# Kernel optimization log

Measured on AMD Instinct MI355X. Metric: run time of the kernel, lower is better.

Reference implementation:

```python
import jax, jax.numpy as jnp
import numpy as np
from jax import lax

IN_CH, OUT_CH, K, STYLE_DIM = 512, 512, 3, 512
B, H, W = 16, 64, 64
SCALE = 1.0 / np.sqrt(IN_CH * K * K).astype(np.float32)
EPS = 1e-8


def setup_inputs() -> dict:
    key = jax.random.key(0)
    k1, k2, k3, k4 = jax.random.split(key, 4)
    return {
        "x": jax.random.normal(k1, (B, IN_CH, H, W), dtype=jnp.float32),
        "style": jax.random.normal(k2, (B, STYLE_DIM), dtype=jnp.float32),
        "weight": jax.random.normal(k3, (1, OUT_CH, IN_CH, K, K), dtype=jnp.float32),
        "mod_w": jax.random.normal(k4, (IN_CH, STYLE_DIM), dtype=jnp.float32) / np.sqrt(STYLE_DIM),
        "mod_b": jnp.ones((IN_CH,), dtype=jnp.float32),
    }


def reference(x, style, weight, mod_w, mod_b):
    b, cin, h, w = x.shape
    out_ch = weight.shape[1]
    k = weight.shape[-1]
    pad = k // 2
    # style projection: (B, in_channel)
    s = style @ mod_w.T + mod_b
    # modulated weight: (B, out, in, k, k)
    wmod = SCALE * weight * s[:, None, :, None, None]
    # demodulation: rsqrt of sum of squares over (in, kh, kw)
    demod = lax.rsqrt(jnp.sum(wmod * wmod, axis=(2, 3, 4)) + EPS)
    wmod = wmod * demod[:, :, None, None, None]
    # grouped conv with groups = batch
    wflat = wmod.reshape(b * out_ch, cin, k, k)
    xin = x.reshape(1, b * cin, h, w)
    out = lax.conv_general_dilated(
        xin, wflat,
        window_strides=(1, 1),
        padding=[(pad, pad), (pad, pad)],
        dimension_numbers=("NCHW", "OIHW", "NCHW"),
        feature_group_count=b,
    )
    return out.reshape(b, out_ch, h, w)
```

## Files before the change

### kernel.cpp

```cpp
#include <hip/hip_runtime.h>
#include <hip/hip_bf16.h>
#include <cstdint>
#include <cstddef>

typedef __bf16 bf16x8 __attribute__((ext_vector_type(8)));
typedef float f32x4 __attribute__((ext_vector_type(4)));
typedef float f32x16 __attribute__((ext_vector_type(16)));

#define MOD_SCALE 1.4731391e-02f
#define EPSF 1e-8f

__global__ __launch_bounds__(512) void k_style(
    const float* __restrict__ style, const float* __restrict__ mod_w,
    const float* __restrict__ mod_b, float* __restrict__ s)
{
  __shared__ float st[512];
  const int b = blockIdx.x, i = threadIdx.x;
  st[i] = style[b*512 + i];
  __syncthreads();
  const float4* mw = (const float4*)(mod_w + (size_t)i*512);
  float acc = 0.f;
  #pragma unroll 8
  for (int j = 0; j < 128; ++j) {
    float4 v = mw[j];
    acc += v.x*st[4*j] + v.y*st[4*j+1] + v.z*st[4*j+2] + v.w*st[4*j+3];
  }
  s[b*512 + i] = acc + mod_b[i];
}

__global__ __launch_bounds__(256) void k_weight(
    const float* __restrict__ weight, float* __restrict__ w2,
    __hip_bfloat16* __restrict__ Wb)
{
  const int o = blockIdx.x, t = threadIdx.x;
  #pragma unroll
  for (int h = 0; h < 2; ++h) {
    const int i = t + h*256;
    const float* wp = weight + ((size_t)o*512 + i)*9;
    float sq = 0.f;
    #pragma unroll
    for (int kk = 0; kk < 9; ++kk) {
      float v = wp[kk];
      sq += v*v;
      Wb[((size_t)kk*512 + o)*512 + i] = __float2bfloat16(v * MOD_SCALE);
    }
    w2[(size_t)o*512 + i] = sq;
  }
}

__global__ __launch_bounds__(256) void k_demod(
    const float* __restrict__ s, const float* __restrict__ w2,
    float* __restrict__ demod)
{
  __shared__ float s2[512];
  const int b = blockIdx.x, t = threadIdx.x;
  {
    float a = s[b*512 + t];        s2[t]     = a*a;
    float c = s[b*512 + t + 256];  s2[t+256] = c*c;
  }
  __syncthreads();
  #pragma unroll
  for (int h = 0; h < 2; ++h) {
    const int o = t + h*256;
    const float4* wp = (const float4*)(w2 + (size_t)o*512);
    float acc = 0.f;
    #pragma unroll 8
    for (int j = 0; j < 128; ++j) {
      float4 v = wp[j];
      acc += v.x*s2[4*j] + v.y*s2[4*j+1] + v.z*s2[4*j+2] + v.w*s2[4*j+3];
    }
    demod[b*512 + o] = rsqrtf(MOD_SCALE*MOD_SCALE*acc + EPSF);
  }
}

__global__ __launch_bounds__(256) void k_xm(
    const float* __restrict__ x, const float* __restrict__ s,
    __hip_bfloat16* __restrict__ Xm)
{
  __shared__ __hip_bfloat16 T[64][40];
  const int bid = blockIdx.x;
  const int cb = bid & 15, y = (bid >> 4) & 63, b = bid >> 10;
  const int ic0 = cb*32;
  const int t = threadIdx.x;
  const int i = t >> 3, x0 = (t & 7)*8;
  const float sv = s[b*512 + ic0 + i];
  const float4* xp = (const float4*)(x + (size_t)(b*512 + ic0 + i)*4096 + y*64 + x0);
  float4 v0 = xp[0], v1 = xp[1];
  float vals[8] = {v0.x, v0.y, v0.z, v0.w, v1.x, v1.y, v1.z, v1.w};
  #pragma unroll
  for (int j = 0; j < 8; ++j) T[x0+j][i] = __float2bfloat16(vals[j]*sv);

  const float4 z4 = make_float4(0.f, 0.f, 0.f, 0.f);
  if (t < 8) {
    const int side = t >> 2, j = t & 3;
    float4* hz = (float4*)(Xm + (((size_t)(b*66 + (y+1))*66 + side*65)*512 + ic0 + j*8));
    *hz = z4;
  }
  if (y == 0) {
    for (int idx = t; idx < 264; idx += 256) {
      const int px = idx >> 2, j = idx & 3;
      float4* hz = (float4*)(Xm + (((size_t)(b*66 + 0)*66 + px)*512 + ic0 + j*8));
      *hz = z4;
    }
  }
  if (y == 63) {
    for (int idx = t; idx < 264; idx += 256) {
      const int px = idx >> 2, j = idx & 3;
      float4* hz = (float4*)(Xm + (((size_t)(b*66 + 65)*66 + px)*512 + ic0 + j*8));
      *hz = z4;
    }
  }

  __syncthreads();
  const int p = t >> 2, c = (t & 3)*8;
  __hip_bfloat16* dst = Xm + (((size_t)(b*66 + (y+1))*66 + (p+1))*512 + ic0 + c);
  *(float4*)dst = *(const float4*)&T[p][c];
}

#define VMC(n) asm volatile("s_waitcnt vmcnt(" #n ")" ::: "memory")

__global__ __launch_bounds__(512, 2) void k_conv(
    const __hip_bfloat16* __restrict__ Wb,
    const __hip_bfloat16* __restrict__ Xm,
    const float* __restrict__ demod,
    float* __restrict__ out)
{
  __shared__ __hip_bfloat16 lds[2][2][16384];

  const int orig = blockIdx.x;
  const int swz = (orig & 7)*64 + (orig >> 3);
  const int b  = swz >> 5;
  const int nt = (swz & 31) >> 1;
  const int mt = swz & 1;
  const int o0 = mt*256, y0 = nt*4;

  const int tid = threadIdx.x;
  const int l = tid & 63;
  const int w = tid >> 6;
  const int wm = w >> 2;
  const int wn = w & 3;

  const int srow = tid >> 3;
  const int tq   = (tid & 7) ^ (srow & 7);
  const char* WbC = (const char*)Wb;
  const char* XmC = (const char*)Xm;

  const int rowb = ((l >> 5) << 4) | (l & 15);
  const int lb4  = (l >> 4) & 1;
  const int sB   = (l & 7) << 4;

  #define STAGE_A(tau, h, bfi) do { \
    const int kk_ = (tau) >> 3; \
    const int cb_ = ((tau) & 7) << 7; \
    _Pragma("unroll") \
    for (int it_ = 0; it_ < 2; ++it_) { \
      const int R_ = it_*64 + srow; \
      const int gr_ = (R_ & 0x6F) | ((tq & 1) << 4); \
      const int gc_ = ((tq & 6) | ((R_ >> 4) & 1)) << 4; \
      const char* src_ = WbC + (size_t)(kk_*512 + o0 + (h)*128 + gr_)*1024 + cb_ + gc_; \
      __builtin_amdgcn_global_load_lds( \
        (__attribute__((address_space(1))) void*)src_, \
        (__attribute__((address_space(3))) void*)((char*)&lds[bfi][0][0] + (h)*16384 + it_*8192 + w*1024), \
        16, 0, 0); \
    } \
  } while(0)

  #define STAGE_B(tau, h, bfi) do { \
    const int kk_ = (tau) >> 3; \
    const int cb_ = ((tau) & 7) << 7; \
    const int dy_ = kk_/3 - 1, dx_ = kk_ - (kk_/3)*3 - 1; \
    _Pragma("unroll") \
    for (int it_ = 0; it_ < 2; ++it_) { \
      const int R_ = it_*64 + srow; \
      const int gr_ = (R_ & 0x6F) | ((tq & 1) << 4); \
      const int gc_ = ((tq & 6) | ((R_ >> 4) & 1)) << 4; \
      const int py_ = y0 + (h)*2 + (gr_ >> 6) + dy_ + 1; \
      const int px_ = (gr_ & 63) + dx_ + 1; \
      const char* src_ = XmC + ((size_t)((b*66 + py_)*66 + px_))*1024 + cb_ + gc_; \
      __builtin_amdgcn_global_load_lds( \
        (__attribute__((address_space(1))) void*)src_, \
        (__attribute__((address_space(3))) void*)((char*)&lds[bfi][1][0] + (h)*16384 + it_*8192 + w*1024), \
        16, 0, 0); \
    } \
  } while(0)

  #define STAGE_TILE(tau, bfi) do { \
    STAGE_A(tau, 0, bfi); STAGE_A(tau, 1, bfi); \
    STAGE_B(tau, 0, bfi); STAGE_B(tau, 1, bfi); \
  } while(0)

  #define RDP(p_, av, bv) do { \
    const int kc_ = ((((p_) << 1) | lb4) << 4) ^ sB; \
    _Pragma("unroll") \
    for (int j_ = 0; j_ < 4; ++j_) \
      av[j_] = *(const bf16x8*)(Ab_ + (j_ >> 1)*16384 + wm*8192 + (j_ & 1)*4096 \
                                + rowb*128 + kc_); \
    _Pragma("unroll") \
    for (int nh_ = 0; nh_ < 2; ++nh_) \
      bv[nh_] = *(const bf16x8*)(Bb_ + nh_*16384 + wn*4096 + rowb*128 + kc_); \
  } while(0)

  #define MM(av, bv) do { \
    _Pragma("unroll") \
    for (int j_ = 0; j_ < 4; ++j_) \
      _Pragma("unroll") \
      for (int nh_ = 0; nh_ < 2; ++nh_) \
        acc[j_][nh_] = __builtin_amdgcn_mfma_f32_32x32x16_bf16( \
            av[j_], bv[nh_], acc[j_][nh_], 0, 0, 0); \
  } while(0)

  f32x16 acc[4][2] = {};

  #define TILE(BFI, STG, VMCW, BAR) do { \
    const char* Ab_ = (const char*)&lds[BFI][0][0]; \
    const char* Bb_ = (const char*)&lds[BFI][1][0]; \
    bf16x8 aX_[4], bX_[2], aY_[4], bY_[2]; \
    RDP(0, aX_, bX_); \
    STG; \
    RDP(1, aY_, bY_); \
    MM(aX_, bX_); \
    RDP(2, aX_, bX_); \
    MM(aY_, bY_); \
    RDP(3, aY_, bY_); \
    MM(aX_, bX_); \
    MM(aY_, bY_); \
    VMCW; \
    if (BAR) __builtin_amdgcn_s_barrier(); \
  } while(0)

  STAGE_TILE(0, 0);
  VMC(0);
  __builtin_amdgcn_s_barrier();

  #pragma unroll 1
  for (int tt = 0; tt < 35; ++tt) {
    const int t = tt*2;
    TILE(0, STAGE_TILE(t+1, 1), VMC(0), 1);
    TILE(1, STAGE_TILE(t+2, 0), VMC(0), 1);
  }
  TILE(0, STAGE_TILE(71, 1), VMC(0), 1);
  TILE(1, (void)0, (void)0, 0);

  const int lr = l & 31;
  #pragma unroll
  for (int am = 0; am < 4; ++am) {
    const int om = o0 + (am >> 1)*128 + wm*64 + (am & 1)*32 + ((l >> 5) << 2);
    #pragma unroll
    for (int NH = 0; NH < 2; ++NH) {
      const int nc = NH*128 + wn*32 + lr;
      const int y = y0 + (nc >> 6), xx = nc & 63;
      #pragma unroll
      for (int g = 0; g < 4; ++g) {
        const f32x4 dm = *(const f32x4*)(demod + b*512 + om + 8*g);
        float* op = out + (size_t)(b*512 + om + 8*g)*4096 + y*64 + xx;
        #pragma unroll
        for (int j = 0; j < 4; ++j)
          op[(size_t)j*4096] = acc[am][NH][g*4 + j] * dm[j];
      }
    }
  }
  #undef TILE
  #undef MM
  #undef RDP
  #undef STAGE_TILE
  #undef STAGE_A
  #undef STAGE_B
}

extern "C" void kernel_launch(void* const* d_in, const int* in_sizes, int n_in,
                              void* d_out, int out_size, void* d_ws, size_t ws_size,
                              hipStream_t stream)
{
  const float* x      = (const float*)d_in[0];
  const float* style  = (const float*)d_in[1];
  const float* weight = (const float*)d_in[2];
  const float* mod_w  = (const float*)d_in[3];
  const float* mod_b  = (const float*)d_in[4];
  float* out = (float*)d_out;

  char* ws = (char*)d_ws;
  float* s            = (float*)(ws);
  float* demod        = (float*)(ws + 32768);
  float* w2           = (float*)(ws + 65536);
  __hip_bfloat16* Wb  = (__hip_bfloat16*)(ws + 1114112);
  __hip_bfloat16* Xm  = (__hip_bfloat16*)(ws + 5832704);

  k_style <<<16,    512, 0, stream>>>(style, mod_w, mod_b, s);
  k_weight<<<512,   256, 0, stream>>>(weight, w2, Wb);
  k_demod <<<16,    256, 0, stream>>>(s, w2, demod);
  k_xm    <<<16384, 256, 0, stream>>>(x, s, Xm);
  k_conv  <<<512,   512, 0, stream>>>(Wb, Xm, demod, out);
}
```

Baseline: 393.0 us.

## Use 4 waves per conv block with 128x128 per-wave tiles and precomputed offsets

Cuts the conv kernel from 8 waves to 4 per block, so each wave now computes a 128x128 output sub-tile (4x4 MFMA 32x32 accumulators) instead of 64x64. Per-wave register reuse of A and B fragments goes up and the LDS read traffic per MFMA goes down. Global-to-LDS staging addresses are now precomputed per thread, and each thread issues four loads per half-tile. The cost is heavier register pressure (256 accumulator floats per lane), lower occupancy with launch bounds (256,1), and less latency hiding.

```diff
diff --git a/kernel.cpp b/kernel.cpp
--- a/kernel.cpp
+++ b/kernel.cpp
@@ -119,7 +119,7 @@
 
 #define VMC(n) asm volatile("s_waitcnt vmcnt(" #n ")" ::: "memory")
 
-__global__ __launch_bounds__(512, 2) void k_conv(
+__global__ __launch_bounds__(256, 1) void k_conv(
     const __hip_bfloat16* __restrict__ Wb,
     const __hip_bfloat16* __restrict__ Xm,
     const float* __restrict__ demod,
@@ -137,54 +137,51 @@
   const int tid = threadIdx.x;
   const int l = tid & 63;
   const int w = tid >> 6;
-  const int wm = w >> 2;
-  const int wn = w & 3;
+  const int wm = w >> 1;
+  const int wn = w & 1;
 
   const int srow = tid >> 3;
   const int tq   = (tid & 7) ^ (srow & 7);
   const char* WbC = (const char*)Wb;
   const char* XmC = (const char*)Xm;
 
+  int aoff[4], boff[4];
+  #pragma unroll
+  for (int it = 0; it < 4; ++it) {
+    const int R  = it*32 + srow;
+    const int gr = (R & 0x6F) | ((tq & 1) << 4);
+    const int gc = ((tq & 6) | ((R >> 4) & 1)) << 4;
+    aoff[it] = (o0 + gr)*1024 + gc;
+    boff[it] = (((b*66 + y0 + 1 + (gr >> 6))*66) + (gr & 63) + 1)*1024 + gc;
+  }
+
   const int rowb = ((l >> 5) << 4) | (l & 15);
   const int lb4  = (l >> 4) & 1;
   const int sB   = (l & 7) << 4;
 
   #define STAGE_A(tau, h, bfi) do { \
-    const int kk_ = (tau) >> 3; \
-    const int cb_ = ((tau) & 7) << 7; \
-    _Pragma("unroll") \
-    for (int it_ = 0; it_ < 2; ++it_) { \
-      const int R_ = it_*64 + srow; \
-      const int gr_ = (R_ & 0x6F) | ((tq & 1) << 4); \
-      const int gc_ = ((tq & 6) | ((R_ >> 4) & 1)) << 4; \
-      const char* src_ = WbC + (size_t)(kk_*512 + o0 + (h)*128 + gr_)*1024 + cb_ + gc_; \
+    const int u_ = ((tau) >> 3)*524288 + (h)*131072 + (((tau) & 7) << 7); \
+    _Pragma("unroll") \
+    for (int it_ = 0; it_ < 4; ++it_) \
       __builtin_amdgcn_global_load_lds( \
-        (__attribute__((address_space(1))) void*)src_, \
-        (__attribute__((address_space(3))) void*)((char*)&lds[bfi][0][0] + (h)*16384 + it_*8192 + w*1024), \
+        (__attribute__((address_space(1))) void*)(WbC + u_ + aoff[it_]), \
+        (__attribute__((address_space(3))) void*)((char*)&lds[bfi][0][0] + (h)*16384 + it_*4096 + w*1024), \
         16, 0, 0); \
-    } \
   } while(0)
 
   #define STAGE_B(tau, h, bfi) do { \
     const int kk_ = (tau) >> 3; \
-    const int cb_ = ((tau) & 7) << 7; \
     const int dy_ = kk_/3 - 1, dx_ = kk_ - (kk_/3)*3 - 1; \
-    _Pragma("unroll") \
-    for (int it_ = 0; it_ < 2; ++it_) { \
-      const int R_ = it_*64 + srow; \
-      const int gr_ = (R_ & 0x6F) | ((tq & 1) << 4); \
-      const int gc_ = ((tq & 6) | ((R_ >> 4) & 1)) << 4; \
-      const int py_ = y0 + (h)*2 + (gr_ >> 6) + dy_ + 1; \
-      const int px_ = (gr_ & 63) + dx_ + 1; \
-      const char* src_ = XmC + ((size_t)((b*66 + py_)*66 + px_))*1024 + cb_ + gc_; \
+    const int u_ = (((h)*2 + dy_)*66 + dx_)*1024 + (((tau) & 7) << 7); \
+    _Pragma("unroll") \
+    for (int it_ = 0; it_ < 4; ++it_) \
       __builtin_amdgcn_global_load_lds( \
-        (__attribute__((address_space(1))) void*)src_, \
-        (__attribute__((address_space(3))) void*)((char*)&lds[bfi][1][0] + (h)*16384 + it_*8192 + w*1024), \
+        (__attribute__((address_space(1))) void*)(XmC + u_ + boff[it_]), \
+        (__attribute__((address_space(3))) void*)((char*)&lds[bfi][1][0] + (h)*16384 + it_*4096 + w*1024), \
         16, 0, 0); \
-    } \
-  } while(0)
-
-  #define STAGE_TILE(tau, bfi) do { \
+  } while(0)
+
+  #define STG_TILE(tau, bfi) do { \
     STAGE_A(tau, 0, bfi); STAGE_A(tau, 1, bfi); \
     STAGE_B(tau, 0, bfi); STAGE_B(tau, 1, bfi); \
   } while(0)
@@ -192,29 +189,28 @@
   #define RDP(p_, av, bv) do { \
     const int kc_ = ((((p_) << 1) | lb4) << 4) ^ sB; \
     _Pragma("unroll") \
-    for (int j_ = 0; j_ < 4; ++j_) \
-      av[j_] = *(const bf16x8*)(Ab_ + (j_ >> 1)*16384 + wm*8192 + (j_ & 1)*4096 \
-                                + rowb*128 + kc_); \
-    _Pragma("unroll") \
-    for (int nh_ = 0; nh_ < 2; ++nh_) \
-      bv[nh_] = *(const bf16x8*)(Bb_ + nh_*16384 + wn*4096 + rowb*128 + kc_); \
+    for (int mi_ = 0; mi_ < 4; ++mi_) \
+      av[mi_] = *(const bf16x8*)(Ab_ + wm*16384 + mi_*4096 + rowb*128 + kc_); \
+    _Pragma("unroll") \
+    for (int ni_ = 0; ni_ < 4; ++ni_) \
+      bv[ni_] = *(const bf16x8*)(Bb_ + wn*16384 + ni_*4096 + rowb*128 + kc_); \
   } while(0)
 
   #define MM(av, bv) do { \
     _Pragma("unroll") \
-    for (int j_ = 0; j_ < 4; ++j_) \
+    for (int mi_ = 0; mi_ < 4; ++mi_) \
       _Pragma("unroll") \
-      for (int nh_ = 0; nh_ < 2; ++nh_) \
-        acc[j_][nh_] = __builtin_amdgcn_mfma_f32_32x32x16_bf16( \
-            av[j_], bv[nh_], acc[j_][nh_], 0, 0, 0); \
-  } while(0)
-
-  f32x16 acc[4][2] = {};
+      for (int ni_ = 0; ni_ < 4; ++ni_) \
+        acc[mi_][ni_] = __builtin_amdgcn_mfma_f32_32x32x16_bf16( \
+            av[mi_], bv[ni_], acc[mi_][ni_], 0, 0, 0); \
+  } while(0)
+
+  f32x16 acc[4][4] = {};
 
   #define TILE(BFI, STG, VMCW, BAR) do { \
     const char* Ab_ = (const char*)&lds[BFI][0][0]; \
     const char* Bb_ = (const char*)&lds[BFI][1][0]; \
-    bf16x8 aX_[4], bX_[2], aY_[4], bY_[2]; \
+    bf16x8 aX_[4], bX_[4], aY_[4], bY_[4]; \
     RDP(0, aX_, bX_); \
     STG; \
     RDP(1, aY_, bY_); \
@@ -228,26 +224,25 @@
     if (BAR) __builtin_amdgcn_s_barrier(); \
   } while(0)
 
-  STAGE_TILE(0, 0);
+  STG_TILE(0, 0);
   VMC(0);
   __builtin_amdgcn_s_barrier();
 
   #pragma unroll 1
-  for (int tt = 0; tt < 35; ++tt) {
-    const int t = tt*2;
-    TILE(0, STAGE_TILE(t+1, 1), VMC(0), 1);
-    TILE(1, STAGE_TILE(t+2, 0), VMC(0), 1);
-  }
-  TILE(0, STAGE_TILE(71, 1), VMC(0), 1);
+  for (int t = 0; t < 71; ++t) {
+    const int bfi = t & 1;
+    if (bfi == 0) { TILE(0, STG_TILE(t+1, 1), VMC(0), 1); }
+    else          { TILE(1, STG_TILE(t+1, 0), VMC(0), 1); }
+  }
   TILE(1, (void)0, (void)0, 0);
 
   const int lr = l & 31;
   #pragma unroll
-  for (int am = 0; am < 4; ++am) {
-    const int om = o0 + (am >> 1)*128 + wm*64 + (am & 1)*32 + ((l >> 5) << 2);
+  for (int mi = 0; mi < 4; ++mi) {
+    const int om = o0 + wm*128 + mi*32 + ((l >> 5) << 2);
     #pragma unroll
-    for (int NH = 0; NH < 2; ++NH) {
-      const int nc = NH*128 + wn*32 + lr;
+    for (int ni = 0; ni < 4; ++ni) {
+      const int nc = wn*128 + ni*32 + lr;
       const int y = y0 + (nc >> 6), xx = nc & 63;
       #pragma unroll
       for (int g = 0; g < 4; ++g) {
@@ -255,14 +250,14 @@
         float* op = out + (size_t)(b*512 + om + 8*g)*4096 + y*64 + xx;
         #pragma unroll
         for (int j = 0; j < 4; ++j)
-          op[(size_t)j*4096] = acc[am][NH][g*4 + j] * dm[j];
+          op[(size_t)j*4096] = acc[mi][ni][g*4 + j] * dm[j];
       }
     }
   }
   #undef TILE
   #undef MM
   #undef RDP
-  #undef STAGE_TILE
+  #undef STG_TILE
   #undef STAGE_A
   #undef STAGE_B
 }
@@ -289,5 +284,5 @@
   k_weight<<<512,   256, 0, stream>>>(weight, w2, Wb);
   k_demod <<<16,    256, 0, stream>>>(s, w2, demod);
   k_xm    <<<16384, 256, 0, stream>>>(x, s, Xm);
-  k_conv  <<<512,   512, 0, stream>>>(Wb, Xm, demod, out);
-}
+  k_conv  <<<512,   256, 0, stream>>>(Wb, Xm, demod, out);
+}
```

Result: slower. 1.133 ms (+188.2%).
